# Optimization experiments

Hardware: AMD Instinct MI355X
Metric: run time of the kernel (lower is better)

Reference implementation:

```python
import jax, jax.numpy as jnp
import numpy as np

HEADS = 8
DIM_HEAD = 64
QUERY_DIM = 320
INNER = HEADS * DIM_HEAD
B = 1
N = 2304          # 48*48 latent pixels
HS = WS = 48
SCALE = DIM_HEAD ** -0.5
ATTN_MATRIX_SCALE = 1.5   # injection_config['T']


def setup_inputs() -> dict:
    key = jax.random.key(0)
    ks = jax.random.split(key, 10)
    f = lambda k, s: jax.random.normal(k, s, dtype=jnp.float32)
    return {
        'x': f(ks[0], (B, N, QUERY_DIM)),
        'Wq': f(ks[1], (QUERY_DIM, INNER)) * 0.05,
        'Wo': f(ks[2], (INNER, QUERY_DIM)) * 0.05,
        'bo': jnp.zeros((QUERY_DIM,), jnp.float32),
        'q_injected': f(ks[3], (B * HEADS, N, DIM_HEAD)),
        'k_injected': f(ks[4], (B * HEADS, N, DIM_HEAD)),
        'v_injected': f(ks[5], (B * HEADS, N, DIM_HEAD)),
        'cnt_k_injected': f(ks[6], (B * HEADS, N, DIM_HEAD)),
        'cnt_v_injected': f(ks[7], (B * HEADS, N, DIM_HEAD)),
        'mask': jax.random.uniform(ks[8], (HS, WS), dtype=jnp.float32),
    }


def _split_heads(t):
    # 'b n (h d) -> (b h) n d'
    b, n, _ = t.shape
    return t.reshape(b, n, HEADS, DIM_HEAD).transpose(0, 2, 1, 3).reshape(b * HEADS, n, DIM_HEAD)


def reference(x, Wq, Wo, bo, q_injected, k_injected, v_injected,
              cnt_k_injected, cnt_v_injected, mask):
    # --- q/k/v with injection (b=1 so torch.cat([.]*b) is identity) ---
    q_in = q_injected                          # (bh, N, d)
    q_ = _split_heads(x @ Wq)                  # to_q(x) -> (bh, N, d)
    q = 0.5 * q_in + 0.5 * q_                  # blended query
    k = k_injected
    v = v_injected
    q_cnt, k_cnt, v_cnt = q_in, cnt_k_injected, cnt_v_injected

    # --- get_batch_sim: content-content similarity (b=1 => rearrange is identity) ---
    cc_sim = jnp.einsum('hid,hjd->hij', q_cnt, k_cnt) * SCALE     # (h, N, N)

    # --- get_batch_sim_with_mask ---
    sim = jnp.einsum('hid,hjd->hij', q, k) * (ATTN_MATRIX_SCALE * SCALE)  # (h, N, N)
    sim_r = sim.reshape(HEADS, HS, WS, N)
    cc_r = cc_sim.reshape(HEADS, HS, WS, N)
    max_sim = jnp.einsum('hid,hjd->hij', q_cnt, k)                # delta_q x delta_k (=self.k)
    max_sim_r = max_sim.reshape(HEADS, HS, WS, N)
    min_cc = jnp.min(cc_r, axis=3, keepdims=True)                 # (h, HS, WS, 1)
    max_ms = jnp.max(max_sim_r, axis=3, keepdims=True)            # (h, HS, WS, 1)

    # binary-threshold the mask, flip sign, bilinear-resize to (HS, WS)
    m = jnp.where(mask < 0.5, -1.0, jnp.where(mask > 0.5, 1.0, mask)) * -1.0
    m = jax.image.resize(m[None, None], (1, 1, HS, WS), method='bilinear')
    m = m.reshape(1, HS, WS, 1)

    gvm = (min_cc - max_ms) * m                                   # gradual_vanished_mask
    sim = (sim_r + gvm).reshape(HEADS, N, N)                      # rows [:WS] == all rows here

    # B=1 => the view/permute/reshape block is identity: sim, cc_sim are (h, N, N)
    # concatenated softmax over style keys and content keys
    cat_sim = jnp.concatenate([sim, cc_sim], axis=2)              # (h, N, 2N)
    cat_attn = jax.nn.softmax(cat_sim, axis=-1)
    cat_v = jnp.concatenate([v, v_cnt], axis=1)                   # (h, 2N, d)
    cat_out = jnp.einsum('hij,hjd->hid', cat_attn, cat_v)         # (h, N, d)

    # 'h (b n) d -> b n (h d)' with b=1
    out = cat_out.transpose(1, 0, 2).reshape(B, N, INNER)
    return out @ Wo + bo
```

## Files before the change

kernel.cpp:

```cpp
#include <hip/hip_runtime.h>
#include <math.h>

#define HEADS 8
#define NTOK  2304
#define DH    64
#define QD    320
#define INNER 512
#define NSPLIT 4
#define TPS   18

typedef _Float16 f16;
typedef f16  f16x4 __attribute__((ext_vector_type(4)));
typedef f16  f16x8 __attribute__((ext_vector_type(8)));
typedef float f32x4 __attribute__((ext_vector_type(4)));

#define MFMA(a,b,c) __builtin_amdgcn_mfma_f32_16x16x32_f16((a),(b),(c),0,0,0)

#define GLDS(gp, lp) __builtin_amdgcn_global_load_lds(                      \
    (const __attribute__((address_space(1))) void*)(gp),                    \
    (__attribute__((address_space(3))) void*)(lp), 16, 0, 0)

#if __has_builtin(__builtin_amdgcn_exp2f)
#define EXP2(x) __builtin_amdgcn_exp2f(x)
#else
#define EXP2(x) exp2f(x)
#endif

#define LOG2E 1.44269504f

static __device__ __forceinline__ unsigned pkrtz(float a, float b) {
#if __has_builtin(__builtin_amdgcn_cvt_pkrtz)
  return __builtin_bit_cast(unsigned, __builtin_amdgcn_cvt_pkrtz(a, b));
#else
  union { f16 h[2]; unsigned u; } c;
  c.h[0] = (f16)a; c.h[1] = (f16)b;
  return c.u;
#endif
}

__global__ __launch_bounds__(256) void prep_all(
    const float* __restrict__ qi, const float* __restrict__ ki,
    const float* __restrict__ kc, const float* __restrict__ x,
    const float* __restrict__ v,  const float* __restrict__ vc,
    const float* __restrict__ Wq, const float* __restrict__ Wo,
    f16* __restrict__ oq, f16* __restrict__ ok, f16* __restrict__ okc,
    f16* __restrict__ ox, f16* __restrict__ vt, f16* __restrict__ vct,
    f16* __restrict__ WqT, f16* __restrict__ WoT)
{
  __shared__ float T[64][65];
  const int bid = blockIdx.x;
  const int tid = threadIdx.x;

  if (bid < 2088) {
    int i = bid * 256 + tid;
    const float* src; f16* dst; float s = 1.0f; int off;
    if (i < 147456)      { src = qi; dst = oq;  off = i; }
    else if (i < 294912) { src = ki; dst = ok;  off = i - 147456; }
    else if (i < 442368) { src = kc; dst = okc; off = i - 294912; s = 0.125f * LOG2E; }
    else                 { src = x;  dst = ox;  off = i - 442368; }
    float4 a = reinterpret_cast<const float4*>(src)[off * 2];
    float4 b = reinterpret_cast<const float4*>(src)[off * 2 + 1];
    f16x8 o;
    o[0] = (f16)(a.x * s); o[1] = (f16)(a.y * s);
    o[2] = (f16)(a.z * s); o[3] = (f16)(a.w * s);
    o[4] = (f16)(b.x * s); o[5] = (f16)(b.y * s);
    o[6] = (f16)(b.z * s); o[7] = (f16)(b.w * s);
    *reinterpret_cast<f16x8*>(&dst[(size_t)off * 8]) = o;
  } else if (bid < 2664) {
    int t = bid - 2088;
    int z = t / 288, rem = t % 288;
    int h = rem / 36, nt = rem % 36;
    const float* src = z ? vc : v;
    f16* dst = z ? vct : vt;
    const int n0 = nt * 64;
    const size_t base = ((size_t)h * NTOK + n0) * DH;
    for (int it = 0; it < 4; ++it) {
      int idx = tid + it * 256;
      int n = idx >> 4, d0 = (idx & 15) * 4;
      float4 a = *reinterpret_cast<const float4*>(&src[base + (size_t)n * DH + d0]);
      T[n][d0] = a.x; T[n][d0 + 1] = a.y; T[n][d0 + 2] = a.z; T[n][d0 + 3] = a.w;
    }
    __syncthreads();
    for (int it = 0; it < 2; ++it) {
      int idx = tid + it * 256;
      int d = idx >> 3, c0 = (idx & 7) * 8;
      f16x8 o;
      #pragma unroll
      for (int i = 0; i < 8; ++i) o[i] = (f16)T[c0 + i][d];
      *reinterpret_cast<f16x8*>(&dst[(size_t)(h * 64 + d) * NTOK + n0 + c0]) = o;
    }
  } else {
    int t = bid - 2664;
    int z = t / 40, b = t % 40;
    const float* src = z ? Wo : Wq;
    f16* dst = z ? WoT : WqT;
    const int R = z ? INNER : QD;
    const int C = z ? QD : INNER;
    const int ctiles = C >> 6;
    const int rt = b / ctiles, ct = b % ctiles;
    for (int it = 0; it < 4; ++it) {
      int idx = tid + it * 256;
      int r = idx >> 4, c4 = (idx & 15) * 4;
      float4 a = *reinterpret_cast<const float4*>(&src[(size_t)(rt * 64 + r) * C + ct * 64 + c4]);
      T[r][c4] = a.x; T[r][c4 + 1] = a.y; T[r][c4 + 2] = a.z; T[r][c4 + 3] = a.w;
    }
    __syncthreads();
    for (int it = 0; it < 4; ++it) {
      int idx = tid + it * 256;
      int c = idx >> 4, r4 = (idx & 15) * 4;
      f16x4 o;
      #pragma unroll
      for (int i = 0; i < 4; ++i) o[i] = (f16)T[r4 + i][c];
      *reinterpret_cast<f16x4*>(&dst[(size_t)(ct * 64 + c) * R + rt * 64 + r4]) = o;
    }
  }
}

__global__ __launch_bounds__(256) void qblend_mfma(
    const f16* __restrict__ x16, const f16* __restrict__ WqT,
    const float* __restrict__ qinj, f16* __restrict__ qhat)
{
  const int qt = blockIdx.x, h = blockIdx.y;
  const int n0 = qt * 32;
  const int tid = threadIdx.x;
  const int w = tid >> 6, l = tid & 63, lq = l & 15, lk = l >> 4;
  const int qsub = w & 1, ch = w >> 1;
  f32x4 acc[2] = {};
  const f16* arow = x16 + (size_t)(n0 + qsub * 16 + lq) * QD;
  #pragma unroll
  for (int ks = 0; ks < 10; ++ks) {
    f16x8 a = *reinterpret_cast<const f16x8*>(&arow[ks * 32 + lk * 8]);
    #pragma unroll
    for (int df = 0; df < 2; ++df) {
      const f16* brow = WqT + (size_t)(h * 64 + ch * 32 + df * 16 + lq) * QD;
      f16x8 b = *reinterpret_cast<const f16x8*>(&brow[ks * 32 + lk * 8]);
      acc[df] = MFMA(a, b, acc[df]);
    }
  }
  const float sc = 0.09375f * LOG2E;
  #pragma unroll
  for (int df = 0; df < 2; ++df)
    #pragma unroll
    for (int r = 0; r < 4; ++r) {
      int n = n0 + qsub * 16 + lk * 4 + r;
      int d = ch * 32 + df * 16 + lq;
      size_t idx = ((size_t)h * NTOK + n) * DH + d;
      qhat[idx] = (f16)(sc * (qinj[idx] + acc[df][r]));
    }
}

__global__ __launch_bounds__(128, 2) void attn_f16p(
    const f16* __restrict__ qhat, const f16* __restrict__ qc16,
    const f16* __restrict__ k16,  const f16* __restrict__ kc16,
    const f16* __restrict__ vt16, const f16* __restrict__ vct16,
    f16* __restrict__ partO, float* __restrict__ partS)
{
  __shared__ __align__(16) f16 smem[2][2][2048];
  __shared__ __align__(16) f16 pbuf[2][640];

  const int bid = blockIdx.x;
  const int h    = bid & 7;
  const int strm = (bid >> 3) & 1;
  const int sp   = (bid >> 4) & 3;
  const int qt   = bid >> 6;
  const int tid = threadIdx.x;
  const int w = tid >> 6, l = tid & 63;
  const int lq = l & 15, lk = l >> 4;
  const size_t hb = (size_t)h * NTOK * DH;
  const int row0 = qt * 96 + w * 48 + lq;

  f16x8 qh0[2], qh1[2], qh2[2], qc0[2], qc1[2], qc2[2];
  {
    const size_t qr0 = hb + (size_t)row0 * DH;
    #pragma unroll
    for (int ks = 0; ks < 2; ++ks) {
      const int o = ks * 32 + lk * 8;
      qc0[ks] = *reinterpret_cast<const f16x8*>(&qc16[qr0 + o]);
      qc1[ks] = *reinterpret_cast<const f16x8*>(&qc16[qr0 + 16 * DH + o]);
      qc2[ks] = *reinterpret_cast<const f16x8*>(&qc16[qr0 + 32 * DH + o]);
      if (!strm) {
        qh0[ks] = *reinterpret_cast<const f16x8*>(&qhat[qr0 + o]);
        qh1[ks] = *reinterpret_cast<const f16x8*>(&qhat[qr0 + 16 * DH + o]);
        qh2[ks] = *reinterpret_cast<const f16x8*>(&qhat[qr0 + 32 * DH + o]);
      } else { qh0[ks] = qc0[ks]; qh1[ks] = qc1[ks]; qh2[ks] = qc2[ks]; }
    }
  }

  const int krow = tid >> 3;
  const int ksw  = ((tid & 7) ^ (krow & 7)) * 8;
  const int vrow = tid >> 2;
  const int voff = (tid & 3) * 8;
  const f16* gK = (strm ? kc16 : k16) + hb;
  const f16* gV = (strm ? vct16 : vt16) + (size_t)h * DH * NTOK;
  const int lb0 = __builtin_amdgcn_readfirstlane((tid & 64) * 8);
  const int lb1 = 1024 + lb0;

  #define STAGE(nb, j0)                                                      \
    do {                                                                     \
      GLDS(gK + (size_t)((j0) + krow) * 64 + ksw,        &smem[nb][0][lb0]); \
      GLDS(gK + (size_t)((j0) + 16 + krow) * 64 + ksw,   &smem[nb][0][lb1]); \
      GLDS(gV + (size_t)vrow * NTOK + (j0) + voff,       &smem[nb][1][lb0]); \
      GLDS(gV + (size_t)(32 + vrow) * NTOK + (j0) + voff,&smem[nb][1][lb1]); \
    } while (0)

  const int swz = (lq & 7) * 8;
  int xo[2];
  #pragma unroll
  for (int ks = 0; ks < 2; ++ks) xo[ks] = ((ks * 32 + lk * 8) ^ swz);

  float S0 = 0.f, S1 = 0.f, S2 = 0.f;
  float ax0, ax1, ax2;
  ax0 = ax1 = ax2 = strm ? INFINITY : -INFINITY;
  f32x4 O0[4] = {}, O1_[4] = {}, O2_[4] = {};
  f16* Pq = &pbuf[w][0];

  auto SMX = [&](const f32x4* s, float& Sl) -> f16x8 {
    float p0 = EXP2(s[0][0]), p1 = EXP2(s[0][1]);
    float p2 = EXP2(s[0][2]), p3 = EXP2(s[0][3]);
    float p4 = EXP2(s[1][0]), p5 = EXP2(s[1][1]);
    float p6 = EXP2(s[1][2]), p7 = EXP2(s[1][3]);
    Sl += ((p0 + p1) + (p2 + p3)) + ((p4 + p5) + (p6 + p7));
    uint2 wA, wB;
    wA.x = pkrtz(p0, p1); wA.y = pkrtz(p2, p3);
    wB.x = pkrtz(p4, p5); wB.y = pkrtz(p6, p7);
    *reinterpret_cast<uint2*>(Pq + lq * 40 + lk * 4)      = wA;
    *reinterpret_cast<uint2*>(Pq + lq * 40 + 16 + lk * 4) = wB;
    return *reinterpret_cast<const f16x8*>(Pq + lq * 40 + lk * 8);
  };

  const int jb = sp * (TPS * 32);
  STAGE(0, jb);
  asm volatile("s_waitcnt vmcnt(0)" ::: "memory");
  __builtin_amdgcn_sched_barrier(0);
  __builtin_amdgcn_s_barrier();
  __builtin_amdgcn_sched_barrier(0);

  int cur = 0;
  for (int t = 0; t < TPS; ++t) {
    if (t + 1 < TPS) STAGE(cur ^ 1, jb + (t + 1) * 32);

    const f16* Kb = &smem[cur][0][0];
    const f16* Vb = &smem[cur][1][0];

    f32x4 sA[2] = {}, sB[2] = {}, sC[2] = {};
    __builtin_amdgcn_s_setprio(1);
    if (!strm) {
      float m3A = -INFINITY, m3B = -INFINITY, m3C = -INFINITY;
      #pragma unroll
      for (int jf = 0; jf < 2; ++jf) {
        f32x4 tA = {}, tB = {}, tC = {};
        const int rb = (jf * 16 + lq) * 64;
        #pragma unroll
        for (int ks = 0; ks < 2; ++ks) {
          f16x8 aK = *reinterpret_cast<const f16x8*>(&Kb[rb + xo[ks]]);
          sA[jf] = MFMA(aK, qh0[ks], sA[jf]);
          sB[jf] = MFMA(aK, qh1[ks], sB[jf]);
          sC[jf] = MFMA(aK, qh2[ks], sC[jf]);
          tA = MFMA(aK, qc0[ks], tA);
          tB = MFMA(aK, qc1[ks], tB);
          tC = MFMA(aK, qc2[ks], tC);
        }
        m3A = fmaxf(m3A, fmaxf(fmaxf(tA[0], tA[1]), fmaxf(tA[2], tA[3])));
        m3B = fmaxf(m3B, fmaxf(fmaxf(tB[0], tB[1]), fmaxf(tB[2], tB[3])));
        m3C = fmaxf(m3C, fmaxf(fmaxf(tC[0], tC[1]), fmaxf(tC[2], tC[3])));
      }
      ax0 = fmaxf(ax0, m3A); ax1 = fmaxf(ax1, m3B); ax2 = fmaxf(ax2, m3C);
    } else {
      #pragma unroll
      for (int jf = 0; jf < 2; ++jf) {
        const int rb = (jf * 16 + lq) * 64;
        #pragma unroll
        for (int ks = 0; ks < 2; ++ks) {
          f16x8 aK = *reinterpret_cast<const f16x8*>(&Kb[rb + xo[ks]]);
          sA[jf] = MFMA(aK, qc0[ks], sA[jf]);
          sB[jf] = MFMA(aK, qc1[ks], sB[jf]);
          sC[jf] = MFMA(aK, qc2[ks], sC[jf]);
        }
      }
      ax0 = fminf(ax0, fminf(fminf(fminf(sA[0][0], sA[0][1]), fminf(sA[0][2], sA[0][3])),
                             fminf(fminf(sA[1][0], sA[1][1]), fminf(sA[1][2], sA[1][3]))));
      ax1 = fminf(ax1, fminf(fminf(fminf(sB[0][0], sB[0][1]), fminf(sB[0][2], sB[0][3])),
                             fminf(fminf(sB[1][0], sB[1][1]), fminf(sB[1][2], sB[1][3]))));
      ax2 = fminf(ax2, fminf(fminf(fminf(sC[0][0], sC[0][1]), fminf(sC[0][2], sC[0][3])),
                             fminf(fminf(sC[1][0], sC[1][1]), fminf(sC[1][2], sC[1][3]))));
    }
    __builtin_amdgcn_s_setprio(0);

    f16x8 pbA = SMX(sA, S0);
    f16x8 pbB = SMX(sB, S1);
    f16x8 pbC = SMX(sC, S2);

    __builtin_amdgcn_s_setprio(1);
    #pragma unroll
    for (int df = 0; df < 4; ++df) {
      f16x8 aV = *reinterpret_cast<const f16x8*>(&Vb[(df * 16 + lq) * 32 + lk * 8]);
      O0[df]  = MFMA(aV, pbA, O0[df]);
      O1_[df] = MFMA(aV, pbB, O1_[df]);
      O2_[df] = MFMA(aV, pbC, O2_[df]);
    }
    __builtin_amdgcn_s_setprio(0);

    asm volatile("s_waitcnt vmcnt(0)" ::: "memory");
    __builtin_amdgcn_sched_barrier(0);
    __builtin_amdgcn_s_barrier();
    __builtin_amdgcn_sched_barrier(0);
    cur ^= 1;
  }

  S0 += __shfl_xor(S0, 16); S0 += __shfl_xor(S0, 32);
  S1 += __shfl_xor(S1, 16); S1 += __shfl_xor(S1, 32);
  S2 += __shfl_xor(S2, 16); S2 += __shfl_xor(S2, 32);
  if (!strm) {
    ax0 = fmaxf(ax0, __shfl_xor(ax0, 16)); ax0 = fmaxf(ax0, __shfl_xor(ax0, 32));
    ax1 = fmaxf(ax1, __shfl_xor(ax1, 16)); ax1 = fmaxf(ax1, __shfl_xor(ax1, 32));
    ax2 = fmaxf(ax2, __shfl_xor(ax2, 16)); ax2 = fmaxf(ax2, __shfl_xor(ax2, 32));
  } else {
    ax0 = fminf(ax0, __shfl_xor(ax0, 16)); ax0 = fminf(ax0, __shfl_xor(ax0, 32));
    ax1 = fminf(ax1, __shfl_xor(ax1, 16)); ax1 = fminf(ax1, __shfl_xor(ax1, 32));
    ax2 = fminf(ax2, __shfl_xor(ax2, 16)); ax2 = fminf(ax2, __shfl_xor(ax2, 32));
  }
  {
    const size_t u = (size_t)((strm * NSPLIT + sp) * 8 + h);
    f16* p0 = partO + (u * NTOK + (size_t)row0) * 64;
    f16* p1 = p0 + (size_t)16 * 64;
    f16* p2 = p0 + (size_t)32 * 64;
    #pragma unroll
    for (int df = 0; df < 4; ++df) {
      uint2 w0, w1, w2;
      w0.x = pkrtz(O0[df][0],  O0[df][1]);  w0.y = pkrtz(O0[df][2],  O0[df][3]);
      w1.x = pkrtz(O1_[df][0], O1_[df][1]); w1.y = pkrtz(O1_[df][2], O1_[df][3]);
      w2.x = pkrtz(O2_[df][0], O2_[df][1]); w2.y = pkrtz(O2_[df][2], O2_[df][3]);
      *reinterpret_cast<uint2*>(p0 + df * 16 + lk * 4) = w0;
      *reinterpret_cast<uint2*>(p1 + df * 16 + lk * 4) = w1;
      *reinterpret_cast<uint2*>(p2 + df * 16 + lk * 4) = w2;
    }
    if (lk == 0) {
      float* s0 = partS + (u * NTOK + (size_t)row0) * 2;
      s0[0] = S0; s0[1] = ax0;
      s0[32] = S1; s0[33] = ax1;
      s0[64] = S2; s0[65] = ax2;
    }
  }
  #undef STAGE
}

__global__ __launch_bounds__(256) void merge8(
    const f16* __restrict__ partO, const float* __restrict__ partS,
    const float* __restrict__ mask, f16* __restrict__ mid)
{
  const int qt = blockIdx.x, h = blockIdx.y;
  const int tid = threadIdx.x;
  const int r = tid >> 2, ds = (tid & 3) * 16;
  const int n = qt * 64 + r;

  float S1 = 0.f, S2 = 0.f, mx = -INFINITY, mn = INFINITY;
  #pragma unroll
  for (int s = 0; s < NSPLIT; ++s) {
    const float* a = partS + ((size_t)((0 * NSPLIT + s) * 8 + h) * NTOK + n) * 2;
    const float* b = partS + ((size_t)((1 * NSPLIT + s) * 8 + h) * NTOK + n) * 2;
    S1 += a[0]; mx = fmaxf(mx, a[1]);
    S2 += b[0]; mn = fminf(mn, b[1]);
  }

  float mv = mask[n];
  float mm = (mv < 0.5f) ? 1.0f : (mv > 0.5f ? -1.0f : -mv);
  float gvm = (mn - mx * LOG2E) * mm;
  float A1 = gvm;
  float Mf = fmaxf(A1, 0.0f);
  float w1 = exp2f(A1 - Mf), w2 = exp2f(-Mf);
  float inv = 1.0f / (w1 * S1 + w2 * S2);

  float o1[16] = {}, o2[16] = {};
  #pragma unroll
  for (int s = 0; s < NSPLIT; ++s) {
    const f16* a = partO + ((size_t)((0 * NSPLIT + s) * 8 + h) * NTOK + n) * 64 + ds;
    const f16* b = partO + ((size_t)((1 * NSPLIT + s) * 8 + h) * NTOK + n) * 64 + ds;
    f16x8 a0 = *reinterpret_cast<const f16x8*>(a);
    f16x8 a1 = *reinterpret_cast<const f16x8*>(a + 8);
    f16x8 b0 = *reinterpret_cast<const f16x8*>(b);
    f16x8 b1 = *reinterpret_cast<const f16x8*>(b + 8);
    #pragma unroll
    for (int j = 0; j < 8; ++j) {
      o1[j]     += (float)a0[j];
      o1[8 + j] += (float)a1[j];
      o2[j]     += (float)b0[j];
      o2[8 + j] += (float)b1[j];
    }
  }
  f16 ov[16];
  #pragma unroll
  for (int j = 0; j < 16; ++j)
    ov[j] = (f16)((w1 * o1[j] + w2 * o2[j]) * inv);
  f16* dst = mid + (size_t)n * INNER + h * 64 + ds;
  *reinterpret_cast<f16x8*>(dst)     = *reinterpret_cast<f16x8*>(&ov[0]);
  *reinterpret_cast<f16x8*>(dst + 8) = *reinterpret_cast<f16x8*>(&ov[8]);
}

__global__ __launch_bounds__(64) void out_mfma(
    const f16* __restrict__ mid, const f16* __restrict__ WoT,
    const float* __restrict__ bo, float* __restrict__ out)
{
  const int n0 = blockIdx.x * 16;
  const int o0 = blockIdx.y * 64;
  const int l = threadIdx.x, lq = l & 15, lk = l >> 4;
  f32x4 acc[4] = {};
  const f16* arow = mid + (size_t)(n0 + lq) * INNER;
  #pragma unroll
  for (int ks = 0; ks < 16; ++ks) {
    f16x8 a = *reinterpret_cast<const f16x8*>(&arow[ks * 32 + lk * 8]);
    #pragma unroll
    for (int df = 0; df < 4; ++df) {
      f16x8 b = *reinterpret_cast<const f16x8*>(
          &WoT[(size_t)(o0 + df * 16 + lq) * INNER + ks * 32 + lk * 8]);
      acc[df] = MFMA(a, b, acc[df]);
    }
  }
  #pragma unroll
  for (int df = 0; df < 4; ++df) {
    float bb = bo[o0 + df * 16 + lq];
    #pragma unroll
    for (int r = 0; r < 4; ++r) {
      int n = n0 + lk * 4 + r;
      out[(size_t)n * QD + o0 + df * 16 + lq] = acc[df][r] + bb;
    }
  }
}

extern "C" void kernel_launch(void* const* d_in, const int* in_sizes, int n_in,
                              void* d_out, int out_size, void* d_ws, size_t ws_size,
                              hipStream_t stream) {
  const float* x    = (const float*)d_in[0];
  const float* Wq   = (const float*)d_in[1];
  const float* Wo   = (const float*)d_in[2];
  const float* bo   = (const float*)d_in[3];
  const float* qinj = (const float*)d_in[4];
  const float* kinj = (const float*)d_in[5];
  const float* vinj = (const float*)d_in[6];
  const float* kcnt = (const float*)d_in[7];
  const float* vcnt = (const float*)d_in[8];
  const float* mask = (const float*)d_in[9];
  float* out = (float*)d_out;

  const size_t T = (size_t)HEADS * NTOK * DH;
  f16* qhat = (f16*)d_ws;
  f16* qc16 = qhat + T;
  f16* k16  = qc16 + T;
  f16* kc16 = k16  + T;
  f16* vt16 = kc16 + T;
  f16* vct16= vt16 + T;
  f16* mid  = vct16 + T;
  f16* x16  = mid;
  f16* WqT  = mid + 737280;
  f16* WoT  = mid + T;
  f16* partO = WoT + 163840;
  float* partS = (float*)(partO + (size_t)64 * NTOK * 64);

  prep_all   <<<2744, 256, 0, stream>>>(qinj, kinj, kcnt, x, vinj, vcnt, Wq, Wo,
                                        qc16, k16, kc16, x16, vt16, vct16, WqT, WoT);
  qblend_mfma<<<dim3(72, 8), 256, 0, stream>>>(x16, WqT, qinj, qhat);
  attn_f16p  <<<1536, 128, 0, stream>>>(qhat, qc16, k16, kc16, vt16, vct16,
                                        partO, partS);
  merge8     <<<dim3(36, 8), 256, 0, stream>>>(partO, partS, mask, mid);
  out_mfma   <<<dim3(144, 5), 64, 0, stream>>>(mid, WoT, bo, out);
}
```

Before: 78.64 us.

## Fuse Q projection into prep kernel and split attention keys six ways

The q-blend GEMM is folded into the prep kernel as extra blocks. These blocks read fp32 x and Wq directly, transpose Wq tiles through double-buffered LDS and convert to fp16 on the fly, which removes the x/WqT conversion pass and one kernel launch. The key-split count of the attention kernel goes from 4 to 6 (12 tiles per split), giving 2304 blocks for better CU occupancy at the cost of more partial outputs to merge. The merge kernel is adjusted to the 6-way split with a linear grid. A risk is that qhat is now produced in the same launch that reads qi, and block ordering inside prep is relied on implicitly, though attention still runs in a later launch.

```diff
diff --git a/kernel.cpp b/kernel.cpp
--- a/kernel.cpp
+++ b/kernel.cpp
@@ -6,8 +6,8 @@
 #define DH    64
 #define QD    320
 #define INNER 512
-#define NSPLIT 4
-#define TPS   18
+#define NSPLIT 6
+#define TPS   12
 
 typedef _Float16 f16;
 typedef f16  f16x4 __attribute__((ext_vector_type(4)));
@@ -44,20 +44,20 @@
     const float* __restrict__ v,  const float* __restrict__ vc,
     const float* __restrict__ Wq, const float* __restrict__ Wo,
     f16* __restrict__ oq, f16* __restrict__ ok, f16* __restrict__ okc,
-    f16* __restrict__ ox, f16* __restrict__ vt, f16* __restrict__ vct,
-    f16* __restrict__ WqT, f16* __restrict__ WoT)
+    f16* __restrict__ vt, f16* __restrict__ vct,
+    f16* __restrict__ WoT, f16* __restrict__ qhat)
 {
   __shared__ float T[64][65];
+  __shared__ __align__(16) f16 qT[2][2560];
   const int bid = blockIdx.x;
   const int tid = threadIdx.x;
 
-  if (bid < 2088) {
+  if (bid < 1728) {
     int i = bid * 256 + tid;
     const float* src; f16* dst; float s = 1.0f; int off;
     if (i < 147456)      { src = qi; dst = oq;  off = i; }
     else if (i < 294912) { src = ki; dst = ok;  off = i - 147456; }
-    else if (i < 442368) { src = kc; dst = okc; off = i - 294912; s = 0.125f * LOG2E; }
-    else                 { src = x;  dst = ox;  off = i - 442368; }
+    else                 { src = kc; dst = okc; off = i - 294912; s = 0.125f * LOG2E; }
     float4 a = reinterpret_cast<const float4*>(src)[off * 2];
     float4 b = reinterpret_cast<const float4*>(src)[off * 2 + 1];
     f16x8 o;
@@ -66,8 +66,8 @@
     o[4] = (f16)(b.x * s); o[5] = (f16)(b.y * s);
     o[6] = (f16)(b.z * s); o[7] = (f16)(b.w * s);
     *reinterpret_cast<f16x8*>(&dst[(size_t)off * 8]) = o;
-  } else if (bid < 2664) {
-    int t = bid - 2088;
+  } else if (bid < 2304) {
+    int t = bid - 1728;
     int z = t / 288, rem = t % 288;
     int h = rem / 36, nt = rem % 36;
     const float* src = z ? vc : v;
@@ -89,19 +89,15 @@
       for (int i = 0; i < 8; ++i) o[i] = (f16)T[c0 + i][d];
       *reinterpret_cast<f16x8*>(&dst[(size_t)(h * 64 + d) * NTOK + n0 + c0]) = o;
     }
-  } else {
-    int t = bid - 2664;
-    int z = t / 40, b = t % 40;
-    const float* src = z ? Wo : Wq;
-    f16* dst = z ? WoT : WqT;
-    const int R = z ? INNER : QD;
-    const int C = z ? QD : INNER;
+  } else if (bid < 2344) {
+    int b2 = bid - 2304;
+    const int R = INNER, C = QD;
     const int ctiles = C >> 6;
-    const int rt = b / ctiles, ct = b % ctiles;
+    const int rt = b2 / ctiles, ct = b2 % ctiles;
     for (int it = 0; it < 4; ++it) {
       int idx = tid + it * 256;
       int r = idx >> 4, c4 = (idx & 15) * 4;
-      float4 a = *reinterpret_cast<const float4*>(&src[(size_t)(rt * 64 + r) * C + ct * 64 + c4]);
+      float4 a = *reinterpret_cast<const float4*>(&Wo[(size_t)(rt * 64 + r) * C + ct * 64 + c4]);
       T[r][c4] = a.x; T[r][c4 + 1] = a.y; T[r][c4 + 2] = a.z; T[r][c4 + 3] = a.w;
     }
     __syncthreads();
@@ -111,42 +107,65 @@
       f16x4 o;
       #pragma unroll
       for (int i = 0; i < 4; ++i) o[i] = (f16)T[r4 + i][c];
-      *reinterpret_cast<f16x4*>(&dst[(size_t)(ct * 64 + c) * R + rt * 64 + r4]) = o;
-    }
-  }
-}
-
-__global__ __launch_bounds__(256) void qblend_mfma(
-    const f16* __restrict__ x16, const f16* __restrict__ WqT,
-    const float* __restrict__ qinj, f16* __restrict__ qhat)
-{
-  const int qt = blockIdx.x, h = blockIdx.y;
-  const int n0 = qt * 32;
-  const int tid = threadIdx.x;
-  const int w = tid >> 6, l = tid & 63, lq = l & 15, lk = l >> 4;
-  const int qsub = w & 1, ch = w >> 1;
-  f32x4 acc[2] = {};
-  const f16* arow = x16 + (size_t)(n0 + qsub * 16 + lq) * QD;
-  #pragma unroll
-  for (int ks = 0; ks < 10; ++ks) {
-    f16x8 a = *reinterpret_cast<const f16x8*>(&arow[ks * 32 + lk * 8]);
-    #pragma unroll
-    for (int df = 0; df < 2; ++df) {
-      const f16* brow = WqT + (size_t)(h * 64 + ch * 32 + df * 16 + lq) * QD;
-      f16x8 b = *reinterpret_cast<const f16x8*>(&brow[ks * 32 + lk * 8]);
-      acc[df] = MFMA(a, b, acc[df]);
-    }
-  }
-  const float sc = 0.09375f * LOG2E;
-  #pragma unroll
-  for (int df = 0; df < 2; ++df)
-    #pragma unroll
-    for (int r = 0; r < 4; ++r) {
-      int n = n0 + qsub * 16 + lk * 4 + r;
-      int d = ch * 32 + df * 16 + lq;
-      size_t idx = ((size_t)h * NTOK + n) * DH + d;
-      qhat[idx] = (f16)(sc * (qinj[idx] + acc[df][r]));
-    }
+      *reinterpret_cast<f16x4*>(&WoT[(size_t)(ct * 64 + c) * R + rt * 64 + r4]) = o;
+    }
+  } else {
+    int b = bid - 2344;
+    int qt = b % 72, h = b / 72;
+    const int n0 = qt * 32;
+    const int w = tid >> 6, l = tid & 63, lq = l & 15, lk = l >> 4;
+    const int qsub = w & 1, ch = w >> 1;
+    const int kk = tid >> 3, c8 = (tid & 7) * 8;
+    f32x4 acc[2] = {};
+    {
+      const float* wr = Wq + (size_t)kk * INNER + h * 64 + c8;
+      float4 a0 = *reinterpret_cast<const float4*>(wr);
+      float4 a1 = *reinterpret_cast<const float4*>(wr + 4);
+      #pragma unroll
+      for (int j = 0; j < 4; ++j) {
+        qT[0][(c8 + j) * 40 + kk]     = (f16)(&a0.x)[j];
+        qT[0][(c8 + 4 + j) * 40 + kk] = (f16)(&a1.x)[j];
+      }
+    }
+    __syncthreads();
+    #pragma unroll
+    for (int ks = 0; ks < 10; ++ks) {
+      if (ks + 1 < 10) {
+        const float* wr = Wq + (size_t)((ks + 1) * 32 + kk) * INNER + h * 64 + c8;
+        float4 a0 = *reinterpret_cast<const float4*>(wr);
+        float4 a1 = *reinterpret_cast<const float4*>(wr + 4);
+        #pragma unroll
+        for (int j = 0; j < 4; ++j) {
+          qT[(ks + 1) & 1][(c8 + j) * 40 + kk]     = (f16)(&a0.x)[j];
+          qT[(ks + 1) & 1][(c8 + 4 + j) * 40 + kk] = (f16)(&a1.x)[j];
+        }
+      }
+      const float* xr = x + (size_t)(n0 + qsub * 16 + lq) * QD + ks * 32 + lk * 8;
+      float4 u0 = *reinterpret_cast<const float4*>(xr);
+      float4 u1 = *reinterpret_cast<const float4*>(xr + 4);
+      f16x8 af;
+      af[0] = (f16)u0.x; af[1] = (f16)u0.y; af[2] = (f16)u0.z; af[3] = (f16)u0.w;
+      af[4] = (f16)u1.x; af[5] = (f16)u1.y; af[6] = (f16)u1.z; af[7] = (f16)u1.w;
+      const f16* bb = &qT[ks & 1][0];
+      #pragma unroll
+      for (int df = 0; df < 2; ++df) {
+        f16x8 bf = *reinterpret_cast<const f16x8*>(
+            &bb[(ch * 32 + df * 16 + lq) * 40 + lk * 8]);
+        acc[df] = MFMA(af, bf, acc[df]);
+      }
+      __syncthreads();
+    }
+    const float scq = 0.09375f * LOG2E;
+    #pragma unroll
+    for (int df = 0; df < 2; ++df)
+      #pragma unroll
+      for (int r = 0; r < 4; ++r) {
+        int n = n0 + qsub * 16 + lk * 4 + r;
+        int d = ch * 32 + df * 16 + lq;
+        size_t idx = ((size_t)h * NTOK + n) * DH + d;
+        qhat[idx] = (f16)(scq * (qi[idx] + acc[df][r]));
+      }
+  }
 }
 
 __global__ __launch_bounds__(128, 2) void attn_f16p(
@@ -161,8 +180,9 @@
   const int bid = blockIdx.x;
   const int h    = bid & 7;
   const int strm = (bid >> 3) & 1;
-  const int sp   = (bid >> 4) & 3;
-  const int qt   = bid >> 6;
+  const int r6   = bid >> 4;
+  const int sp   = r6 % 6;
+  const int qt   = r6 / 6;
   const int tid = threadIdx.x;
   const int w = tid >> 6, l = tid & 63;
   const int lq = l & 15, lk = l >> 4;
@@ -344,11 +364,11 @@
   #undef STAGE
 }
 
-__global__ __launch_bounds__(256) void merge8(
+__global__ __launch_bounds__(256) void merge6(
     const f16* __restrict__ partO, const float* __restrict__ partS,
     const float* __restrict__ mask, f16* __restrict__ mid)
 {
-  const int qt = blockIdx.x, h = blockIdx.y;
+  const int h = blockIdx.x & 7, qt = blockIdx.x >> 3;
   const int tid = threadIdx.x;
   const int r = tid >> 2, ds = (tid & 3) * 16;
   const int n = qt * 64 + r;
@@ -449,17 +469,14 @@
   f16* vt16 = kc16 + T;
   f16* vct16= vt16 + T;
   f16* mid  = vct16 + T;
-  f16* x16  = mid;
-  f16* WqT  = mid + 737280;
   f16* WoT  = mid + T;
   f16* partO = WoT + 163840;
-  float* partS = (float*)(partO + (size_t)64 * NTOK * 64);
-
-  prep_all   <<<2744, 256, 0, stream>>>(qinj, kinj, kcnt, x, vinj, vcnt, Wq, Wo,
-                                        qc16, k16, kc16, x16, vt16, vct16, WqT, WoT);
-  qblend_mfma<<<dim3(72, 8), 256, 0, stream>>>(x16, WqT, qinj, qhat);
-  attn_f16p  <<<1536, 128, 0, stream>>>(qhat, qc16, k16, kc16, vt16, vct16,
-                                        partO, partS);
-  merge8     <<<dim3(36, 8), 256, 0, stream>>>(partO, partS, mask, mid);
-  out_mfma   <<<dim3(144, 5), 64, 0, stream>>>(mid, WoT, bo, out);
-}
+  float* partS = (float*)(partO + (size_t)96 * NTOK * 64);
+
+  prep_all  <<<2920, 256, 0, stream>>>(qinj, kinj, kcnt, x, vinj, vcnt, Wq, Wo,
+                                       qc16, k16, kc16, vt16, vct16, WoT, qhat);
+  attn_f16p <<<2304, 128, 0, stream>>>(qhat, qc16, k16, kc16, vt16, vct16,
+                                       partO, partS);
+  merge6    <<<288, 256, 0, stream>>>(partO, partS, mask, mid);
+  out_mfma  <<<dim3(144, 5), 64, 0, stream>>>(mid, WoT, bo, out);
+}
```

After: 87.19 us. 10.9% more time.
